# Kernel optimization log

Measured on AMD Instinct MI355X. Metric: run time of the kernel, lower is better.

## Reference

```python
import jax, jax.numpy as jnp
import numpy as np

SOS = 1
H = 1024
E = 512
V = 32000


def setup_inputs() -> dict:
    key = jax.random.key(0)
    ks = jax.random.split(key, 16)
    B, T_enc, T = 32, 128, 64
    s = 1.0 / np.sqrt(H)
    inp = {
        'encoder_outputs': jax.random.normal(ks[0], (B, T_enc, H), jnp.float32),
        'encoder_hidden': jax.random.normal(ks[1], (1, B, H), jnp.float32),
        'encoder_cell': jax.random.normal(ks[2], (1, B, H), jnp.float32),
        'target_tensor': jax.random.randint(ks[3], (B, T), 0, V),
        'emb_table': jax.random.normal(ks[4], (V, E), jnp.float32) * 0.02,
        'Wa': jax.random.normal(ks[5], (H, H), jnp.float32) * s,
        'Ua': jax.random.normal(ks[6], (H, H), jnp.float32) * s,
        'Va_w': jax.random.normal(ks[7], (1, H), jnp.float32) * s,
        'Va_b': jnp.zeros((1,), jnp.float32),
        'W_ih': jax.random.normal(ks[8], (4 * H, E + H), jnp.float32) * s,
        'W_hh': jax.random.normal(ks[9], (4 * H, H), jnp.float32) * s,
        'b_ih': jnp.zeros((4 * H,), jnp.float32),
        'b_hh': jnp.zeros((4 * H,), jnp.float32),
        'fc_w': jax.random.normal(ks[10], (V, H), jnp.float32) * s,
        'fc_b': jnp.zeros((V,), jnp.float32),
    }
    return inp


def reference(encoder_outputs, encoder_hidden, encoder_cell, target_tensor,
              emb_table, Wa, Ua, Va_w, Va_b, W_ih, W_hh, b_ih, b_hh, fc_w, fc_b):
    B, T = target_tensor.shape
    # padding_idx=0: embedding row 0 is zeros
    emb_table = emb_table.at[0].set(0.0)
    enc_Ua = jnp.einsum('bth,kh->btk', encoder_outputs, Ua)  # precompute Ua(enc)
    # teacher forcing always: inputs are [SOS, target[:, :-1]], shape [T, B]
    tok_seq = jnp.concatenate([jnp.full((B, 1), SOS, target_tensor.dtype),
                               target_tensor[:, :-1]], axis=1).T

    def step(carry, tok):
        h, c = carry  # [B, H]
        emb = emb_table[tok]  # [B, E]
        # Bahdanau attention (query = last-layer hidden)
        q = h @ Wa.T  # [B, H]
        energy = jnp.tanh(q[:, None, :] + enc_Ua)  # [B, T_enc, H]
        scores = jnp.einsum('bth,h->bt', energy, Va_w[0]) + Va_b[0]
        w = jax.nn.softmax(scores, axis=1)
        context = jnp.einsum('bt,bth->bh', w, encoder_outputs)
        x = jnp.concatenate([emb, context], axis=1)  # [B, E+H]
        gates = x @ W_ih.T + b_ih + h @ W_hh.T + b_hh  # [B, 4H], order i,f,g,o
        i, f, g, o = jnp.split(gates, 4, axis=1)
        c = jax.nn.sigmoid(f) * c + jax.nn.sigmoid(i) * jnp.tanh(g)
        h = jax.nn.sigmoid(o) * jnp.tanh(c)
        logp = jax.nn.log_softmax(h @ fc_w.T + fc_b, axis=1)  # [B, V]
        return (h, c), logp

    (h, c), logps = jax.lax.scan(step, (encoder_hidden[0], encoder_cell[0]), tok_seq)
    outputs = jnp.transpose(logps, (1, 0, 2))  # [B, T, V]
    return outputs
```

## Files before the change

### kernel.cpp

```cpp
#include <hip/hip_runtime.h>
#include <math.h>

#define NB 32
#define TE 128
#define NT 64
#define HH 1024
#define EE 512
#define VV 32000
#define GG 4096
#define WQN 5120
#define NBLK 512

typedef __attribute__((ext_vector_type(8))) short bh8;
typedef __attribute__((ext_vector_type(4))) float fx4;
typedef __attribute__((ext_vector_type(4))) unsigned ux4;
typedef __attribute__((ext_vector_type(4))) float fv4;

__device__ __forceinline__ float tanh_fast(float x) {
  float e = __expf(2.f * x);
  return 1.f - 2.f / (e + 1.f);
}
__device__ __forceinline__ float sigf(float x) { return 1.f / (1.f + __expf(-x)); }
__device__ __forceinline__ ushort f2bf(float x) {
  union { float f; unsigned u; } v; v.f = x;
  unsigned r = v.u + 0x7fffu + ((v.u >> 16) & 1u);
  return (ushort)(r >> 16);
}
__device__ __forceinline__ float bf2f(ushort u) {
  return __uint_as_float(((unsigned)u) << 16);
}

__device__ __forceinline__ void st_f32(float* p, float v) {
  __hip_atomic_store(p, v, __ATOMIC_RELAXED, __HIP_MEMORY_SCOPE_AGENT);
}
__device__ __forceinline__ float ld_f32(const float* p) {
  return __hip_atomic_load(p, __ATOMIC_RELAXED, __HIP_MEMORY_SCOPE_AGENT);
}
__device__ __forceinline__ void st_u32(unsigned* p, unsigned v) {
  __hip_atomic_store(p, v, __ATOMIC_RELAXED, __HIP_MEMORY_SCOPE_AGENT);
}
__device__ __forceinline__ unsigned ld_u32(const unsigned* p) {
  return __hip_atomic_load(p, __ATOMIC_RELAXED, __HIP_MEMORY_SCOPE_AGENT);
}

__global__ void k_init(const float* __restrict__ eh, unsigned* __restrict__ h_u32) {
  int i = blockIdx.x * 256 + threadIdx.x;
  float a = eh[i * 2], b = eh[i * 2 + 1];
  h_u32[i] = (unsigned)f2bf(a) | ((unsigned)f2bf(b) << 16);
}

__global__ void k_emb(const int* __restrict__ tgt, const float* __restrict__ etab,
                      ushort* __restrict__ emb_bf) {
  int idx = blockIdx.x * 256 + threadIdx.x;
  int e = idx & (EE - 1);
  int tb = idx >> 9;
  int b = tb & (NB - 1);
  int t = tb >> 5;
  int tok = (t == 0) ? 1 : tgt[b * NT + (t - 1)];
  emb_bf[idx] = (tok == 0) ? (ushort)0 : f2bf(etab[(size_t)tok * EE + e]);
}

__global__ void k_f2b(const float* __restrict__ s, ushort* __restrict__ d, int n4) {
  int i = blockIdx.x * 256 + threadIdx.x;
  if (i >= n4) return;
  float4 v = *(const float4*)(s + (size_t)i * 4);
  *(ushort4*)(d + (size_t)i * 4) = make_ushort4(f2bf(v.x), f2bf(v.y), f2bf(v.z), f2bf(v.w));
}

__global__ void k_f2b_s(const float* __restrict__ s, int ld, int off, int w4,
                        ushort* __restrict__ d, int n) {
  int i = blockIdx.x * 256 + threadIdx.x;
  if (i >= n) return;
  int r = i / w4, c = (i - r * w4) * 4;
  float4 v = *(const float4*)(s + (size_t)r * ld + off + c);
  *(ushort4*)(d + (size_t)r * (w4 * 4) + c) = make_ushort4(f2bf(v.x), f2bf(v.y), f2bf(v.z), f2bf(v.w));
}

__device__ __forceinline__ void stage_pair(const ushort* A, int lda, const ushort* B, int ldb,
    int m0, int n0, int k0, ushort* ldsA, ushort* ldsB, int tid) {
  const int w = tid >> 6;
  const int row = tid >> 2;
  const int kq = (tid & 3) * 8;
  const ushort* ga = A + (size_t)(m0 + row) * lda + k0 + kq;
  const ushort* gb = B + (size_t)(n0 + row) * ldb + k0 + kq;
  ushort* la = ldsA + w * 512;
  ushort* lb = ldsB + w * 512;
  __builtin_amdgcn_global_load_lds((const __attribute__((address_space(1))) void*)ga,
      (__attribute__((address_space(3))) void*)la, 16, 0, 0);
  __builtin_amdgcn_global_load_lds((const __attribute__((address_space(1))) void*)(ga + (size_t)64 * lda),
      (__attribute__((address_space(3))) void*)(la + 2048), 16, 0, 0);
  __builtin_amdgcn_global_load_lds((const __attribute__((address_space(1))) void*)gb,
      (__attribute__((address_space(3))) void*)lb, 16, 0, 0);
  __builtin_amdgcn_global_load_lds((const __attribute__((address_space(1))) void*)(gb + (size_t)64 * ldb),
      (__attribute__((address_space(3))) void*)(lb + 2048), 16, 0, 0);
}

__global__ __launch_bounds__(256) void k_gemm_bf16(
    const ushort* __restrict__ A, int lda,
    const ushort* __restrict__ B, int ldb,
    const float* __restrict__ b1, const float* __restrict__ b2,
    void* __restrict__ Cv, int ldc, int K, int perm, int obf, int swz) {
  __shared__ ushort lds[2][2][4096];
  const int tid = threadIdx.x;
  const int lane = tid & 63, w = tid >> 6;
  int m0, n0;
  if (swz) {
    const int bid = blockIdx.y * gridDim.x + blockIdx.x;
    m0 = (bid & 15) * 128;
    n0 = (bid >> 4) * 128;
  } else {
    m0 = blockIdx.y * 128;
    n0 = blockIdx.x * 128;
  }
  const int wm = (w >> 1) * 64, wn = (w & 1) * 64;
  fx4 acc[4][4] = {};
  stage_pair(A, lda, B, ldb, m0, n0, 0, lds[0][0], lds[0][1], tid);
  __syncthreads();
  const int nk = K >> 5;
  const int ko = (lane >> 4) * 8;
  const int rA = wm + (lane & 15);
  const int rB = wn + (lane & 15);
  for (int ks = 0; ks < nk; ++ks) {
    const int cur = ks & 1;
    if (ks + 1 < nk)
      stage_pair(A, lda, B, ldb, m0, n0, (ks + 1) << 5, lds[cur ^ 1][0], lds[cur ^ 1][1], tid);
    bh8 af[4], bfr[4];
#pragma unroll
    for (int f = 0; f < 4; ++f) {
      af[f]  = *(const bh8*)(&lds[cur][0][(rA + f * 16) * 32 + ko]);
      bfr[f] = *(const bh8*)(&lds[cur][1][(rB + f * 16) * 32 + ko]);
    }
#pragma unroll
    for (int i = 0; i < 4; ++i)
#pragma unroll
      for (int j = 0; j < 4; ++j)
        acc[i][j] = __builtin_amdgcn_mfma_f32_16x16x32_bf16(af[i], bfr[j], acc[i][j], 0, 0, 0);
    __syncthreads();
  }
  float* Cf = (float*)Cv;
  ushort* Cb = (ushort*)Cv;
#pragma unroll
  for (int j = 0; j < 4; ++j) {
    const int col = n0 + wn + j * 16 + (lane & 15);
    const float bv = (b1 ? b1[col] : 0.f) + (b2 ? b2[col] : 0.f);
#pragma unroll
    for (int i = 0; i < 4; ++i) {
      const int mb = m0 + wm + i * 16 + (lane >> 4) * 4;
#pragma unroll
      for (int r = 0; r < 4; ++r) {
        const int m = mb + r;
        const size_t orow = perm ? ((size_t)(m & 31) * 64 + (m >> 5)) : (size_t)m;
        const float v = acc[i][j][r] + bv;
        if (obf) Cb[orow * (size_t)ldc + col] = f2bf(v);
        else     Cf[orow * (size_t)ldc + col] = v;
      }
    }
  }
}

__device__ __forceinline__ void gridbar(unsigned* flags, unsigned* genArr, int lb, unsigned epoch) {
  asm volatile("s_waitcnt vmcnt(0)" ::: "memory");
  __syncthreads();
  const int tid = threadIdx.x;
  if (tid == 0) st_u32(flags + lb * 32, epoch);
  if (lb == 0) {
    while (ld_u32(flags + tid * 32) < epoch) __builtin_amdgcn_s_sleep(1);
    __syncthreads();
    if (tid < 16) st_u32(genArr + tid * 32, epoch);
  } else if (tid == 0) {
    while (ld_u32(genArr + (lb & 15) * 32) < epoch) __builtin_amdgcn_s_sleep(1);
  }
  __syncthreads();
}

__global__ __launch_bounds__(256, 1) void k_recur(
    const ushort* __restrict__ Wqh,
    const ushort* __restrict__ encU,
    const ushort* __restrict__ encW,
    const float*  __restrict__ embG,
    const float*  __restrict__ Va,
    const float*  __restrict__ ec,
    float* __restrict__ hW,
    float* __restrict__ sc,
    unsigned* __restrict__ h_u32,
    ushort* __restrict__ hall,
    unsigned* __restrict__ flags, unsigned* __restrict__ genArr) {
  const int bid = blockIdx.x;
  const int half = bid >> 8;
  const int lb = bid & 255;
  const int hb0 = half * 16;
  unsigned* flagsH = flags + half * (256 * 32);
  unsigned* genH   = genArr + half * (16 * 32);
  const int tid = threadIdx.x;
  const int lane = tid & 63, w = tid >> 6;
  __shared__ float wlds[4][16][33];
  __shared__ float red[128], wt[TE], gp[4][64];
  __shared__ float cpart[8][4][8][8];
  unsigned epoch = 0;

  const int b3 = hb0 + (lb >> 4), u0 = (lb & 15) * 64;
  float c_r = 0.f;
  if (tid < 64) c_r = ec[b3 * HH + u0 + tid];
  const int bb = b3, tc = lb & 15;

  for (int t = 0; t < NT; ++t) {
    if (lb < 160) {
      const int n0 = lb * 32;
      const int kb = w * 256;
      const int r15 = lane & 15, ko = (lane >> 4) * 8;
      const char* hbase0 = (const char*)h_u32 + (size_t)(hb0 + r15) * 2048 + (size_t)(kb + ko) * 2;
      const ushort* B0 = Wqh + (size_t)(n0 + r15) * HH + kb + ko;
      const ushort* B1 = B0 + 16 * HH;
      fx4 a00 = {}, a01 = {};
#pragma unroll
      for (int hf = 0; hf < 2; ++hf) {
        union { ux4 u; bh8 b; } h0[4];
        const char* p0 = hbase0 + hf * 256;
        asm volatile(
          "global_load_dwordx4 %0, %4, off sc0 sc1\n\t"
          "global_load_dwordx4 %1, %4, off offset:64 sc0 sc1\n\t"
          "global_load_dwordx4 %2, %4, off offset:128 sc0 sc1\n\t"
          "global_load_dwordx4 %3, %4, off offset:192 sc0 sc1\n\t"
          "s_waitcnt vmcnt(0)"
          : "=&v"(h0[0].u), "=&v"(h0[1].u), "=&v"(h0[2].u), "=&v"(h0[3].u)
          : "v"(p0));
#pragma unroll
        for (int ks = 0; ks < 4; ++ks) {
          const int k = (hf * 4 + ks) * 32;
          bh8 bv0 = *(const bh8*)(B0 + k);
          bh8 bv1 = *(const bh8*)(B1 + k);
          a00 = __builtin_amdgcn_mfma_f32_16x16x32_bf16(h0[ks].b, bv0, a00, 0, 0, 0);
          a01 = __builtin_amdgcn_mfma_f32_16x16x32_bf16(h0[ks].b, bv1, a01, 0, 0, 0);
        }
      }
      const int rr = (lane >> 4) * 4;
#pragma unroll
      for (int r = 0; r < 4; ++r) {
        wlds[w][rr + r][r15]      = a00[r];
        wlds[w][rr + r][r15 + 16] = a01[r];
      }
      __syncthreads();
      if (tid < 128) {
        const int row = tid >> 3, c0 = (tid & 7) * 4;
        fv4 s4;
        s4.x = wlds[0][row][c0+0] + wlds[1][row][c0+0] + wlds[2][row][c0+0] + wlds[3][row][c0+0];
        s4.y = wlds[0][row][c0+1] + wlds[1][row][c0+1] + wlds[2][row][c0+1] + wlds[3][row][c0+1];
        s4.z = wlds[0][row][c0+2] + wlds[1][row][c0+2] + wlds[2][row][c0+2] + wlds[3][row][c0+2];
        s4.w = wlds[0][row][c0+3] + wlds[1][row][c0+3] + wlds[2][row][c0+3] + wlds[3][row][c0+3];
        asm volatile("global_store_dwordx4 %0, %1, off sc0 sc1"
                     :: "v"(&hW[(size_t)(hb0 + row) * WQN + n0 + c0]), "v"(s4) : "memory");
      }
    }
    gridbar(flagsH, genH, lb, ++epoch);

    {
      union { ux4 u; float f[4]; } q0, q1, q2, q3;
      const float* qp0 = &hW[(size_t)bb * WQN + lane * 8];
      const float* qp1 = &hW[(size_t)bb * WQN + 512 + lane * 8];
      asm volatile(
        "global_load_dwordx4 %0, %4, off sc0 sc1\n\t"
        "global_load_dwordx4 %1, %4, off offset:16 sc0 sc1\n\t"
        "global_load_dwordx4 %2, %5, off sc0 sc1\n\t"
        "global_load_dwordx4 %3, %5, off offset:16 sc0 sc1\n\t"
        "s_waitcnt vmcnt(0)"
        : "=&v"(q0.u), "=&v"(q1.u), "=&v"(q2.u), "=&v"(q3.u)
        : "v"(qp0), "v"(qp1));
      float qr[16], vr[16];
#pragma unroll
      for (int j = 0; j < 4; ++j) {
        qr[j] = q0.f[j]; qr[4 + j] = q1.f[j];
        qr[8 + j] = q2.f[j]; qr[12 + j] = q3.f[j];
      }
#pragma unroll
      for (int c = 0; c < 2; ++c) {
        const int h0 = c * 512 + lane * 8;
        float4 va = *(const float4*)(Va + h0);
        float4 vb = *(const float4*)(Va + h0 + 4);
        vr[c*8+0] = va.x; vr[c*8+1] = va.y; vr[c*8+2] = va.z; vr[c*8+3] = va.w;
        vr[c*8+4] = vb.x; vr[c*8+5] = vb.y; vr[c*8+6] = vb.z; vr[c*8+7] = vb.w;
      }
#pragma unroll
      for (int it = 0; it < 2; ++it) {
        const int tt = tc * 8 + w * 2 + it;
        const ushort* ep = encU + (size_t)(bb * TE + tt) * HH;
        float a = 0.f;
#pragma unroll
        for (int c = 0; c < 2; ++c) {
          bh8 e8 = *(const bh8*)(ep + c * 512 + lane * 8);
#pragma unroll
          for (int j = 0; j < 8; ++j)
            a += tanh_fast(qr[c * 8 + j] + bf2f((ushort)e8[j])) * vr[c * 8 + j];
        }
#pragma unroll
        for (int s2 = 32; s2 > 0; s2 >>= 1) a += __shfl_xor(a, s2);
        if (lane == 0) st_f32(&sc[bb * TE + tt], a);
      }
    }
    gridbar(flagsH, genH, lb, ++epoch);

    {
      const float sv = (tid < TE) ? ld_f32(&sc[b3 * TE + tid]) : -1e30f;
      if (tid < 128) red[tid] = sv;
      __syncthreads();
      for (int st = 64; st > 0; st >>= 1) {
        if (tid < st) red[tid] = fmaxf(red[tid], red[tid + st]);
        __syncthreads();
      }
      const float mx = red[0];
      __syncthreads();
      const float ev = (tid < TE) ? __expf(sv - mx) : 0.f;
      if (tid < 128) { wt[tid] = ev; red[tid] = ev; }
      __syncthreads();
      for (int st = 64; st > 0; st >>= 1) {
        if (tid < st) red[tid] += red[tid + st];
        __syncthreads();
      }
      const float inv = 1.f / red[0];
      __syncthreads();
      const int oct = tid & 7, g = (tid >> 3) & 3, tq = tid >> 5;
      const ushort* base = encW + (size_t)(b3 * TE + tq * 16) * GG + g * 1024 + u0 + oct * 8;
      float a8[8] = {};
#pragma unroll
      for (int j = 0; j < 16; ++j) {
        bh8 e8 = *(const bh8*)(base + (size_t)j * GG);
        const float wv = wt[tq * 16 + j];
#pragma unroll
        for (int q = 0; q < 8; ++q) a8[q] += wv * bf2f((ushort)e8[q]);
      }
#pragma unroll
      for (int q = 0; q < 8; ++q) cpart[tq][g][oct][q] = a8[q];
      __syncthreads();
      {
        const int c = tid & 63, g2 = tid >> 6;
        float s = 0.f;
#pragma unroll
        for (int q = 0; q < 8; ++q) s += cpart[q][g2][c >> 3][c & 7];
        s *= inv;
        const int cl = g2 * 1024 + u0 + c;
        s += embG[(size_t)(t * NB + b3) * GG + cl];
        float hv;
        asm volatile("global_load_dword %0, %1, off sc0 sc1\n\ts_waitcnt vmcnt(0)"
                     : "=&v"(hv) : "v"(&hW[(size_t)b3 * WQN + HH + cl]));
        gp[g2][c] = s + hv;
      }
      __syncthreads();
      if (tid < 64) {
        const float gi = gp[0][tid], gf = gp[1][tid];
        const float gg = gp[2][tid], go = gp[3][tid];
        const float cn = sigf(gf) * c_r + sigf(gi) * tanh_fast(gg);
        c_r = cn;
        const float hn = sigf(go) * tanh_fast(cn);
        const float hn_p = __shfl_xor(hn, 1);
        if ((tid & 1) == 0) {
          const ushort hb = f2bf(hn), hb1 = f2bf(hn_p);
          st_u32(&h_u32[b3 * 512 + ((u0 + tid) >> 1)],
                 (unsigned)hb | ((unsigned)hb1 << 16));
          *(ushort2*)(hall + (size_t)t * (NB * HH) + b3 * HH + u0 + tid) = make_ushort2(hb, hb1);
        }
      }
    }
    gridbar(flagsH, genH, lb, ++epoch);
  }
}

__global__ __launch_bounds__(256) void k_logsoftmax(float* __restrict__ out) {
  const size_t row = blockIdx.x;
  float* p = out + row * VV;
  __shared__ float sm[256], ss[256];
  const int tid = threadIdx.x;
  float m = -1e30f, s = 0.f;
  for (int i = tid; i < (VV / 4); i += 256) {
    float4 x = *(const float4*)(p + (size_t)i * 4);
    float m4 = fmaxf(fmaxf(x.x, x.y), fmaxf(x.z, x.w));
    float nm = fmaxf(m, m4);
    s = s * __expf(m - nm) + __expf(x.x - nm) + __expf(x.y - nm)
        + __expf(x.z - nm) + __expf(x.w - nm);
    m = nm;
  }
  sm[tid] = m; ss[tid] = s;
  __syncthreads();
  for (int st = 128; st > 0; st >>= 1) {
    if (tid < st) {
      float m2 = fmaxf(sm[tid], sm[tid + st]);
      ss[tid] = ss[tid] * __expf(sm[tid] - m2) + ss[tid + st] * __expf(sm[tid + st] - m2);
      sm[tid] = m2;
    }
    __syncthreads();
  }
  float L = sm[0] + logf(ss[0]);
  __syncthreads();
  for (int i = tid; i < (VV / 4); i += 256) {
    float4 x = *(const float4*)(p + (size_t)i * 4);
    x.x -= L; x.y -= L; x.z -= L; x.w -= L;
    *(float4*)(p + (size_t)i * 4) = x;
  }
}

extern "C" void kernel_launch(void* const* d_in, const int* in_sizes, int n_in,
                              void* d_out, int out_size, void* d_ws, size_t ws_size,
                              hipStream_t stream) {
  const float* enc   = (const float*)d_in[0];
  const float* ehid  = (const float*)d_in[1];
  const float* ecell = (const float*)d_in[2];
  const int*   tgt   = (const int*)d_in[3];
  const float* etab  = (const float*)d_in[4];
  const float* Wa    = (const float*)d_in[5];
  const float* Ua    = (const float*)d_in[6];
  const float* Va_w  = (const float*)d_in[7];
  const float* W_ih  = (const float*)d_in[9];
  const float* W_hh  = (const float*)d_in[10];
  const float* b_ih  = (const float*)d_in[11];
  const float* b_hh  = (const float*)d_in[12];
  const float* fc_w  = (const float*)d_in[13];
  const float* fc_b  = (const float*)d_in[14];
  float* out = (float*)d_out;
  float* ws = (float*)d_ws;

  ushort* encW_bf = (ushort*)ws;
  float*  embG    = ws + 8388608;
  ushort* fcw_bf  = (ushort*)ws;
  ushort* Wqh_bf  = (ushort*)(ws + 16777216);
  ushort* encU_bf = (ushort*)(ws + 19398656);
  ushort* enc_bf  = (ushort*)(ws + 21495808);
  ushort* Wihc_bf = (ushort*)(ws + 23592960);
  ushort* Ua_bf   = (ushort*)(ws + 25690112);
  ushort* emb_bf  = (ushort*)(ws + 26214400);
  ushort* WihE_bf = (ushort*)(ws + 26738688);
  float*  hW      = ws + 21495808;
  float*  sc      = ws + 21659648;
  unsigned* h_u32 = (unsigned*)(ws + 21663744);
  unsigned* flags = (unsigned*)(ws + 27300000);
  unsigned* genArr= (unsigned*)(ws + 27316384);
  ushort* hall_bf = (ushort*)(ws + 27787264);

  k_emb<<<4096, 256, 0, stream>>>(tgt, etab, emb_bf);
  k_f2b<<<4096, 256, 0, stream>>>(enc, enc_bf, 1048576);
  k_f2b<<<1024, 256, 0, stream>>>(Ua, Ua_bf, 262144);
  k_f2b<<<1024, 256, 0, stream>>>(Wa, Wqh_bf, 262144);
  k_f2b<<<4096, 256, 0, stream>>>(W_hh, Wqh_bf + 1024 * HH, 1048576);
  k_f2b_s<<<4096, 256, 0, stream>>>(W_ih, 1536, 512, 256, Wihc_bf, 1048576);
  k_f2b_s<<<2048, 256, 0, stream>>>(W_ih, 1536, 0, 128, WihE_bf, 524288);
  k_gemm_bf16<<<dim3(8, 32), 256, 0, stream>>>(enc_bf, HH, Ua_bf, HH, nullptr, nullptr,
                                               encU_bf, HH, HH, 0, 1, 0);
  k_gemm_bf16<<<dim3(32, 32), 256, 0, stream>>>(enc_bf, HH, Wihc_bf, HH, nullptr, nullptr,
                                                encW_bf, GG, HH, 0, 1, 0);
  k_gemm_bf16<<<dim3(32, 16), 256, 0, stream>>>(emb_bf, EE, WihE_bf, EE, b_ih, b_hh,
                                                embG, GG, EE, 0, 0, 0);
  (void)hipMemsetAsync(flags, 0, (512 * 32 + 32 * 32) * sizeof(unsigned), stream);
  k_init<<<64, 256, 0, stream>>>(ehid, h_u32);

  k_recur<<<NBLK, 256, 0, stream>>>(Wqh_bf, encU_bf, encW_bf, embG, Va_w, ecell,
                                    hW, sc, h_u32, hall_bf, flags, genArr);

  k_f2b<<<32000, 256, 0, stream>>>(fc_w, fcw_bf, 8192000);
  k_gemm_bf16<<<dim3(250, 16), 256, 0, stream>>>(hall_bf, HH, fcw_bf, HH, fc_b, nullptr,
                                                 out, VV, HH, 1, 0, 1);
  k_logsoftmax<<<2048, 256, 0, stream>>>(out);
}
```

Baseline: 1.815 ms.

## Split recurrence into four barrier groups and cache logsoftmax rows in registers

The recurrent kernel is repartitioned from two independent groups of 256 blocks (16 batch rows each) into four groups of 128 blocks (8 batch rows each). Each grid barrier now spans fewer blocks, which should cut sync latency on every timestep. The price is that the 160 query/hidden projection tiles no longer divide evenly: some blocks handle two tiles with extra __syncthreads, and half the MFMA rows are wasted. Separately, logsoftmax now uses 1024-thread blocks that keep the row in registers, use wave-shuffle reductions, and skip the second global read.

```diff
diff --git a/kernel.cpp b/kernel.cpp
--- a/kernel.cpp
+++ b/kernel.cpp
@@ -164,7 +164,8 @@
   const int tid = threadIdx.x;
   if (tid == 0) st_u32(flags + lb * 32, epoch);
   if (lb == 0) {
-    while (ld_u32(flags + tid * 32) < epoch) __builtin_amdgcn_s_sleep(1);
+    if (tid < 128)
+      while (ld_u32(flags + tid * 32) < epoch) __builtin_amdgcn_s_sleep(1);
     __syncthreads();
     if (tid < 16) st_u32(genArr + tid * 32, epoch);
   } else if (tid == 0) {
@@ -186,14 +187,14 @@
     ushort* __restrict__ hall,
     unsigned* __restrict__ flags, unsigned* __restrict__ genArr) {
   const int bid = blockIdx.x;
-  const int half = bid >> 8;
-  const int lb = bid & 255;
-  const int hb0 = half * 16;
-  unsigned* flagsH = flags + half * (256 * 32);
-  unsigned* genH   = genArr + half * (16 * 32);
+  const int quarter = bid >> 7;
+  const int lb = bid & 127;
+  const int hb0 = quarter * 8;
+  unsigned* flagsH = flags + quarter * (128 * 32);
+  unsigned* genH   = genArr + quarter * (16 * 32);
   const int tid = threadIdx.x;
   const int lane = tid & 63, w = tid >> 6;
-  __shared__ float wlds[4][16][33];
+  __shared__ float wlds[4][8][33];
   __shared__ float red[128], wt[TE], gp[4][64];
   __shared__ float cpart[8][4][8][8];
   unsigned epoch = 0;
@@ -204,11 +205,12 @@
   const int bb = b3, tc = lb & 15;
 
   for (int t = 0; t < NT; ++t) {
-    if (lb < 160) {
-      const int n0 = lb * 32;
+    for (int tile = lb; tile < 160; tile += 128) {
+      const int n0 = tile * 32;
       const int kb = w * 256;
       const int r15 = lane & 15, ko = (lane >> 4) * 8;
-      const char* hbase0 = (const char*)h_u32 + (size_t)(hb0 + r15) * 2048 + (size_t)(kb + ko) * 2;
+      const char* hbase0 = (const char*)h_u32 + (size_t)(hb0 + (r15 & 7)) * 2048
+                         + (size_t)(kb + ko) * 2;
       const ushort* B0 = Wqh + (size_t)(n0 + r15) * HH + kb + ko;
       const ushort* B1 = B0 + 16 * HH;
       fx4 a00 = {}, a01 = {};
@@ -236,20 +238,21 @@
       const int rr = (lane >> 4) * 4;
 #pragma unroll
       for (int r = 0; r < 4; ++r) {
-        wlds[w][rr + r][r15]      = a00[r];
-        wlds[w][rr + r][r15 + 16] = a01[r];
-      }
-      __syncthreads();
-      if (tid < 128) {
-        const int row = tid >> 3, c0 = (tid & 7) * 4;
-        fv4 s4;
-        s4.x = wlds[0][row][c0+0] + wlds[1][row][c0+0] + wlds[2][row][c0+0] + wlds[3][row][c0+0];
-        s4.y = wlds[0][row][c0+1] + wlds[1][row][c0+1] + wlds[2][row][c0+1] + wlds[3][row][c0+1];
-        s4.z = wlds[0][row][c0+2] + wlds[1][row][c0+2] + wlds[2][row][c0+2] + wlds[3][row][c0+2];
-        s4.w = wlds[0][row][c0+3] + wlds[1][row][c0+3] + wlds[2][row][c0+3] + wlds[3][row][c0+3];
-        asm volatile("global_store_dwordx4 %0, %1, off sc0 sc1"
-                     :: "v"(&hW[(size_t)(hb0 + row) * WQN + n0 + c0]), "v"(s4) : "memory");
-      }
+        const int row = rr + r;
+        if (row < 8) {
+          wlds[w][row][r15]      = a00[r];
+          wlds[w][row][r15 + 16] = a01[r];
+        }
+      }
+      __syncthreads();
+      {
+        const int row = tid >> 5, c0 = tid & 31;
+        float s = (wlds[0][row][c0] + wlds[1][row][c0])
+                + (wlds[2][row][c0] + wlds[3][row][c0]);
+        asm volatile("global_store_dword %0, %1, off sc0 sc1"
+                     :: "v"(&hW[(size_t)(hb0 + row) * WQN + n0 + c0]), "v"(s) : "memory");
+      }
+      __syncthreads();
     }
     gridbar(flagsH, genH, lb, ++epoch);
 
@@ -363,36 +366,48 @@
   }
 }
 
-__global__ __launch_bounds__(256) void k_logsoftmax(float* __restrict__ out) {
+__global__ __launch_bounds__(1024, 1) void k_logsoftmax(float* __restrict__ out) {
   const size_t row = blockIdx.x;
   float* p = out + row * VV;
-  __shared__ float sm[256], ss[256];
   const int tid = threadIdx.x;
+  const int lane = tid & 63, wv = tid >> 6;
+  __shared__ float sm[16], ss[16], bc[2];
+  float4 v[8];
+  const int nj = (tid < 832) ? 8 : 7;
   float m = -1e30f, s = 0.f;
-  for (int i = tid; i < (VV / 4); i += 256) {
-    float4 x = *(const float4*)(p + (size_t)i * 4);
-    float m4 = fmaxf(fmaxf(x.x, x.y), fmaxf(x.z, x.w));
+  for (int j = 0; j < nj; ++j) {
+    v[j] = *(const float4*)(p + (size_t)(j * 1024 + tid) * 4);
+    float m4 = fmaxf(fmaxf(v[j].x, v[j].y), fmaxf(v[j].z, v[j].w));
     float nm = fmaxf(m, m4);
-    s = s * __expf(m - nm) + __expf(x.x - nm) + __expf(x.y - nm)
-        + __expf(x.z - nm) + __expf(x.w - nm);
+    s = s * __expf(m - nm) + __expf(v[j].x - nm) + __expf(v[j].y - nm)
+        + __expf(v[j].z - nm) + __expf(v[j].w - nm);
     m = nm;
   }
-  sm[tid] = m; ss[tid] = s;
+#pragma unroll
+  for (int st = 32; st > 0; st >>= 1) {
+    float mo = __shfl_xor(m, st), so = __shfl_xor(s, st);
+    float m2 = fmaxf(m, mo);
+    s = s * __expf(m - m2) + so * __expf(mo - m2);
+    m = m2;
+  }
+  if (lane == 0) { sm[wv] = m; ss[wv] = s; }
   __syncthreads();
-  for (int st = 128; st > 0; st >>= 1) {
-    if (tid < st) {
-      float m2 = fmaxf(sm[tid], sm[tid + st]);
-      ss[tid] = ss[tid] * __expf(sm[tid] - m2) + ss[tid + st] * __expf(sm[tid + st] - m2);
-      sm[tid] = m2;
-    }
-    __syncthreads();
-  }
-  float L = sm[0] + logf(ss[0]);
+  if (tid == 0) {
+    float M = sm[0], S = ss[0];
+#pragma unroll
+    for (int i = 1; i < 16; ++i) {
+      float m2 = fmaxf(M, sm[i]);
+      S = S * __expf(M - m2) + ss[i] * __expf(sm[i] - m2);
+      M = m2;
+    }
+    bc[0] = M; bc[1] = S;
+  }
   __syncthreads();
-  for (int i = tid; i < (VV / 4); i += 256) {
-    float4 x = *(const float4*)(p + (size_t)i * 4);
+  const float L = bc[0] + logf(bc[1]);
+  for (int j = 0; j < nj; ++j) {
+    float4 x = v[j];
     x.x -= L; x.y -= L; x.z -= L; x.w -= L;
-    *(float4*)(p + (size_t)i * 4) = x;
+    *(float4*)(p + (size_t)(j * 1024 + tid) * 4) = x;
   }
 }
 
@@ -446,7 +461,7 @@
                                                 encW_bf, GG, HH, 0, 1, 0);
   k_gemm_bf16<<<dim3(32, 16), 256, 0, stream>>>(emb_bf, EE, WihE_bf, EE, b_ih, b_hh,
                                                 embG, GG, EE, 0, 0, 0);
-  (void)hipMemsetAsync(flags, 0, (512 * 32 + 32 * 32) * sizeof(unsigned), stream);
+  (void)hipMemsetAsync(flags, 0, (4 * 128 * 32 + 4 * 16 * 32) * sizeof(unsigned), stream);
   k_init<<<64, 256, 0, stream>>>(ehid, h_u32);
 
   k_recur<<<NBLK, 256, 0, stream>>>(Wqh_bf, encU_bf, encW_bf, embG, Va_w, ecell,
@@ -455,5 +470,5 @@
   k_f2b<<<32000, 256, 0, stream>>>(fc_w, fcw_bf, 8192000);
   k_gemm_bf16<<<dim3(250, 16), 256, 0, stream>>>(hall_bf, HH, fcw_bf, HH, fc_b, nullptr,
                                                  out, VV, HH, 1, 0, 1);
-  k_logsoftmax<<<2048, 256, 0, stream>>>(out);
-}
+  k_logsoftmax<<<2048, 1024, 0, stream>>>(out);
+}
```

New measurement: 2.051 ms. +13.0%, slower.
